# Kernel optimization log

Hardware: AMD Instinct MI355X
Metric: run time of the kernel (lower is better)

## Reference

```python
import jax, jax.numpy as jnp
import numpy as np

B, N, C = 4, 2048, 512
H = 8
HD = C // H  # 64
SCALE = HD ** -0.5


def setup_inputs() -> dict:
    key = jax.random.key(0)
    k1, k2, k3 = jax.random.split(key, 3)
    x = jax.random.normal(k1, (B, N, C), dtype=jnp.float32)
    w_qkv = jax.random.normal(k2, (3 * C, C), dtype=jnp.float32) * (C ** -0.5)
    b_qkv = jnp.zeros((3 * C,), dtype=jnp.float32)
    w_proj = jax.random.normal(k3, (C, C), dtype=jnp.float32) * (C ** -0.5)
    b_proj = jnp.zeros((C,), dtype=jnp.float32)
    return {"x": x, "w_qkv": w_qkv, "b_qkv": b_qkv, "w_proj": w_proj, "b_proj": b_proj}


def reference(x, w_qkv, b_qkv, w_proj, b_proj):
    # qkv projection: (B,N,C) @ (C,3C) -> (B,N,3,H,HD) -> (3,B,H,N,HD)
    qkv = (x @ w_qkv.T + b_qkv).reshape(B, N, 3, H, HD).transpose(2, 0, 3, 1, 4)
    q, k, v = qkv[0], qkv[1], qkv[2]
    # scores (B,H,N,N), scale applied after matmul as in the torch source
    attn = jnp.einsum('bhnd,bhmd->bhnm', q, k) * SCALE
    attn = jax.nn.softmax(attn, axis=-1)
    out = jnp.einsum('bhnm,bhmd->bhnd', attn, v)  # (B,H,N,HD)
    out = out.transpose(0, 2, 1, 3).reshape(B, N, C)
    return out @ w_proj.T + b_proj
```

## Files before the change

### kernel.cpp

```cpp
#include <hip/hip_runtime.h>

#define B_ 4
#define N_ 2048
#define C_ 512
#define H_ 8
#define HD_ 64
#define SCALE_ 0.125f
#define QSCALE_ 0.18033688011112042f

typedef __attribute__((ext_vector_type(8))) __bf16 bf16x8;
typedef __attribute__((ext_vector_type(4))) float f32x4;
typedef __attribute__((ext_vector_type(4))) unsigned int u32x4;

__device__ __forceinline__ unsigned short f2bf(float f) {
    unsigned int u = __builtin_bit_cast(unsigned int, f);
    u += 0x7fffu + ((u >> 16) & 1u);
    return (unsigned short)(u >> 16);
}

__device__ __forceinline__ void llds16(const void* g, void* l) {
    __builtin_amdgcn_global_load_lds(
        (const __attribute__((address_space(1))) unsigned int*)g,
        (__attribute__((address_space(3))) unsigned int*)l, 16, 0, 0);
}

__global__ __launch_bounds__(256) void cvt_bf16(const float* __restrict__ in,
                                                unsigned short* __restrict__ out,
                                                int n4) {
    int i = blockIdx.x * 256 + threadIdx.x;
    if (i >= n4) return;
    float4 v = ((const float4*)in)[i];
    ushort4 o;
    o.x = f2bf(v.x); o.y = f2bf(v.y); o.z = f2bf(v.z); o.w = f2bf(v.w);
    ((ushort4*)out)[i] = o;
}

template <int MODE>
__global__ __launch_bounds__(256) void gemm_bt(const unsigned short* __restrict__ A,
                                               const unsigned short* __restrict__ Bw,
                                               const float* __restrict__ bias,
                                               float* __restrict__ Out,
                                               unsigned short* __restrict__ Qb,
                                               unsigned short* __restrict__ Kb,
                                               unsigned short* __restrict__ Vt) {
    constexpr int K = 512;
    __shared__ __align__(16) unsigned char smem[32768];
    unsigned char* sA = smem;
    unsigned char* sB = smem + 16384;

    const int tid = threadIdx.x;
    const int lane = tid & 63;
    const int wave = tid >> 6;
    const int wm = wave >> 1, wn = wave & 1;
    const int m0 = blockIdx.y * 128;
    const int n0 = blockIdx.x * 128;

    f32x4 acc[4][4] = {};

    for (int k0 = 0; k0 < K; k0 += 64) {
#pragma unroll
        for (int i = 0; i < 4; i++) {
            int ci = wave * 4 + i;
            int row = ci * 8 + (lane >> 3);
            int cb = (lane & 7) * 16;
            const unsigned char* ga =
                (const unsigned char*)A + ((size_t)(m0 + row) * K + k0) * 2 + cb;
            const unsigned char* gb =
                (const unsigned char*)Bw + ((size_t)(n0 + row) * K + k0) * 2 + cb;
            llds16(ga, sA + ci * 1024);
            llds16(gb, sB + ci * 1024);
        }
        __syncthreads();
#pragma unroll
        for (int kk = 0; kk < 2; kk++) {
            bf16x8 af[4], bfr[4];
#pragma unroll
            for (int mi = 0; mi < 4; mi++)
                af[mi] = *(const bf16x8*)(sA + (wm * 64 + mi * 16 + (lane & 15)) * 128 +
                                          kk * 64 + (lane >> 4) * 16);
#pragma unroll
            for (int ni = 0; ni < 4; ni++)
                bfr[ni] = *(const bf16x8*)(sB + (wn * 64 + ni * 16 + (lane & 15)) * 128 +
                                           kk * 64 + (lane >> 4) * 16);
#pragma unroll
            for (int mi = 0; mi < 4; mi++)
#pragma unroll
                for (int ni = 0; ni < 4; ni++)
                    acc[mi][ni] = __builtin_amdgcn_mfma_f32_16x16x32_bf16(
                        af[mi], bfr[ni], acc[mi][ni], 0, 0, 0);
        }
        __syncthreads();
    }

    if constexpr (MODE == 0) {
#pragma unroll
        for (int ni = 0; ni < 4; ni++) {
            int c = n0 + wn * 64 + ni * 16 + (lane & 15);
            int sel = c >> 9, h = (c >> 6) & 7, d = c & 63;
            float bv = bias[c];
#pragma unroll
            for (int mi = 0; mi < 4; mi++) {
#pragma unroll
                for (int r = 0; r < 4; r++) {
                    int m = m0 + wm * 64 + mi * 16 + ((lane >> 4) << 2) + r;
                    int b = m >> 11, n = m & (N_ - 1);
                    float fv = acc[mi][ni][r] + bv;
                    if (sel == 0) {
                        Qb[((size_t)(b * H_ + h) * N_ + n) * HD_ + d] = f2bf(fv * QSCALE_);
                    } else if (sel == 1) {
                        Kb[((size_t)(b * H_ + h) * N_ + n) * HD_ + d] = f2bf(fv);
                    } else {
                        Vt[((size_t)(b * H_ + h) * HD_ + d) * (size_t)N_ + n] = f2bf(fv);
                    }
                }
            }
        }
    } else {
#pragma unroll
        for (int ni = 0; ni < 4; ni++) {
            int c = n0 + wn * 64 + ni * 16 + (lane & 15);
            float bv = bias[c];
#pragma unroll
            for (int mi = 0; mi < 4; mi++) {
#pragma unroll
                for (int r = 0; r < 4; r++) {
                    int m = m0 + wm * 64 + mi * 16 + ((lane >> 4) << 2) + r;
                    Out[(size_t)m * C_ + c] = acc[mi][ni][r] + bv;
                }
            }
        }
    }
}

__global__ __launch_bounds__(512, 4) void attn_fwd(const unsigned short* __restrict__ Qb,
                                                   const unsigned short* __restrict__ Kb,
                                                   const unsigned short* __restrict__ Vt,
                                                   unsigned short* __restrict__ AO) {
    __shared__ __align__(16) unsigned char smem[49152];

    const int tid = threadIdx.x, lane = tid & 63, wave = tid >> 6;
    const int bh = blockIdx.y;
    const int q0 = blockIdx.x * 128 + wave * 16;
    const unsigned short* Qh = Qb + (size_t)bh * N_ * HD_;
    const unsigned short* Kh = Kb + (size_t)bh * N_ * HD_;
    const unsigned short* Vh = Vt + (size_t)bh * HD_ * N_;
    unsigned char* sP = smem + 32768 + wave * 2048;

    bf16x8 qf[2];
#pragma unroll
    for (int kk = 0; kk < 2; kk++)
        qf[kk] = *(const bf16x8*)(Qh + (size_t)(q0 + (lane & 15)) * HD_ + kk * 32 +
                                  (lane >> 4) * 8);

    bf16x8 ones;
#pragma unroll
    for (int i = 0; i < 8; i++) ones[i] = (__bf16)1.0f;

    f32x4 o[4] = {};
    f32x4 osum = {};

    const int srow = tid >> 3;
    const int sslot = (tid & 7) * 16;
    const int ssw = (sslot ^ ((srow & 7) << 4));

    {
        u32x4 kreg = *(const u32x4*)((const unsigned char*)Kh + (size_t)srow * 128 + sslot);
        u32x4 vreg = *(const u32x4*)((const unsigned char*)Vh + (size_t)srow * (N_ * 2) + sslot);
        *(u32x4*)(smem + srow * 128 + ssw) = kreg;
        *(u32x4*)(smem + 16384 + srow * 128 + ssw) = vreg;
    }
    __syncthreads();

#pragma unroll 1
    for (int t = 0; t < N_ / 64; t++) {
        unsigned char* bK = smem + (t & 1) * 8192;
        unsigned char* bV = smem + 16384 + (t & 1) * 8192;

        u32x4 kreg, vreg;
        if (t < N_ / 64 - 1) {
            int kv0 = (t + 1) * 64;
            kreg = *(const u32x4*)((const unsigned char*)Kh + (size_t)(kv0 + srow) * 128 + sslot);
            vreg = *(const u32x4*)((const unsigned char*)Vh + (size_t)srow * (N_ * 2) +
                                   kv0 * 2 + sslot);
        }

        f32x4 s[4] = {};
#pragma unroll
        for (int j = 0; j < 4; j++) {
#pragma unroll
            for (int kk = 0; kk < 2; kk++) {
                int krow = j * 16 + (lane & 15);
                bf16x8 bf = *(const bf16x8*)(bK + krow * 128 +
                                             ((kk * 64 + (lane >> 4) * 16) ^
                                              ((krow & 7) << 4)));
                s[j] = __builtin_amdgcn_mfma_f32_16x16x32_bf16(qf[kk], bf, s[j], 0, 0, 0);
            }
        }

#pragma unroll
        for (int j = 0; j < 4; j++)
#pragma unroll
            for (int r = 0; r < 4; r++) {
                float p = __builtin_exp2f(s[j][r]);
                int row = ((lane >> 4) << 2) + r;
                int cb = (j * 16 + (lane & 15)) * 2;
                *(unsigned short*)(sP + row * 128 + (cb ^ ((row & 7) << 4))) = f2bf(p);
            }

#pragma unroll
        for (int kk = 0; kk < 2; kk++) {
            int prow = lane & 15;
            bf16x8 pf = *(const bf16x8*)(sP + prow * 128 +
                                         ((kk * 64 + (lane >> 4) * 16) ^
                                          ((prow & 7) << 4)));
            osum = __builtin_amdgcn_mfma_f32_16x16x32_bf16(pf, ones, osum, 0, 0, 0);
#pragma unroll
            for (int dj = 0; dj < 4; dj++) {
                int vrow = dj * 16 + (lane & 15);
                bf16x8 vf = *(const bf16x8*)(bV + vrow * 128 +
                                             ((kk * 64 + (lane >> 4) * 16) ^
                                              ((vrow & 7) << 4)));
                o[dj] = __builtin_amdgcn_mfma_f32_16x16x32_bf16(pf, vf, o[dj], 0, 0, 0);
            }
        }

        if (t < N_ / 64 - 1) {
            unsigned char* nK = smem + ((t + 1) & 1) * 8192;
            unsigned char* nV = smem + 16384 + ((t + 1) & 1) * 8192;
            *(u32x4*)(nK + srow * 128 + ssw) = kreg;
            *(u32x4*)(nV + srow * 128 + ssw) = vreg;
        }
        __syncthreads();
    }

    const int b = bh >> 3, h = bh & 7;
#pragma unroll
    for (int r = 0; r < 4; r++) {
        float inv = 1.0f / osum[r];
        int n = q0 + ((lane >> 4) << 2) + r;
#pragma unroll
        for (int dj = 0; dj < 4; dj++) {
            int col = h * HD_ + dj * 16 + (lane & 15);
            AO[((size_t)(b * N_ + n)) * C_ + col] = f2bf(o[dj][r] * inv);
        }
    }
}

extern "C" void kernel_launch(void* const* d_in, const int* in_sizes, int n_in,
                              void* d_out, int out_size, void* d_ws, size_t ws_size,
                              hipStream_t stream) {
    const float* x = (const float*)d_in[0];
    const float* w_qkv = (const float*)d_in[1];
    const float* b_qkv = (const float*)d_in[2];
    const float* w_proj = (const float*)d_in[3];
    const float* b_proj = (const float*)d_in[4];
    float* out = (float*)d_out;

    unsigned char* ws = (unsigned char*)d_ws;
    unsigned short* xb = (unsigned short*)ws;
    unsigned short* AO = xb;
    unsigned short* wqb = (unsigned short*)(ws + 8388608);
    unsigned short* wpb = (unsigned short*)(ws + 8388608 + 1572864);
    unsigned short* Vt = (unsigned short*)(ws + 8388608 + 1572864 + 524288);

    unsigned short* Qb = (unsigned short*)d_out;
    unsigned short* Kb = Qb + (size_t)B_ * H_ * N_ * HD_;

    cvt_bf16<<<(B_ * N_ * C_ / 4 + 255) / 256, 256, 0, stream>>>(x, xb, B_ * N_ * C_ / 4);
    cvt_bf16<<<(3 * C_ * C_ / 4 + 255) / 256, 256, 0, stream>>>(w_qkv, wqb, 3 * C_ * C_ / 4);
    cvt_bf16<<<(C_ * C_ / 4 + 255) / 256, 256, 0, stream>>>(w_proj, wpb, C_ * C_ / 4);

    gemm_bt<0><<<dim3(12, 64), 256, 0, stream>>>(xb, wqb, b_qkv, nullptr, Qb, Kb, Vt);
    attn_fwd<<<dim3(16, 32), 512, 0, stream>>>(Qb, Kb, Vt, AO);
    gemm_bt<1><<<dim3(4, 64), 256, 0, stream>>>(AO, wpb, b_proj, out, nullptr, nullptr, nullptr);
}
```

Baseline: 140.0 us.

## Fuse bf16 conversions and store P transposed, read via ds_read_tr

Merges the three fp32-to-bf16 conversion launches into one kernel to cut launch overhead. In attention, the exp'd scores are packed with v_cvt_pk_bf16_f32 and written to LDS as 64-bit stores in a transposed layout, then read back as MFMA A-operands with ds_read_b64_tr_b16. This replaces sixteen scalar 16-bit LDS stores per tile with four vector stores, at the cost of inline asm, explicit waitcnts and scheduling barriers that may limit overlap.

Result: faster. 126.6 us (-9.6%).

```diff
diff --git a/kernel.cpp b/kernel.cpp
--- a/kernel.cpp
+++ b/kernel.cpp
@@ -11,6 +11,7 @@
 typedef __attribute__((ext_vector_type(8))) __bf16 bf16x8;
 typedef __attribute__((ext_vector_type(4))) float f32x4;
 typedef __attribute__((ext_vector_type(4))) unsigned int u32x4;
+typedef __attribute__((ext_vector_type(2))) unsigned int u32x2;
 
 __device__ __forceinline__ unsigned short f2bf(float f) {
     unsigned int u = __builtin_bit_cast(unsigned int, f);
@@ -24,15 +25,25 @@
         (__attribute__((address_space(3))) unsigned int*)l, 16, 0, 0);
 }
 
-__global__ __launch_bounds__(256) void cvt_bf16(const float* __restrict__ in,
-                                                unsigned short* __restrict__ out,
-                                                int n4) {
+__global__ __launch_bounds__(256) void cvt_all(const float* __restrict__ x,
+                                               const float* __restrict__ wq,
+                                               const float* __restrict__ wp,
+                                               unsigned short* __restrict__ xb,
+                                               unsigned short* __restrict__ wqb,
+                                               unsigned short* __restrict__ wpb) {
+    const int NX = B_ * N_ * C_ / 4, NQ = 3 * C_ * C_ / 4, NP = C_ * C_ / 4;
     int i = blockIdx.x * 256 + threadIdx.x;
-    if (i >= n4) return;
-    float4 v = ((const float4*)in)[i];
+    const float4* src;
+    ushort4* dst;
+    int idx;
+    if (i < NX) { src = (const float4*)x; dst = (ushort4*)xb; idx = i; }
+    else if (i < NX + NQ) { src = (const float4*)wq; dst = (ushort4*)wqb; idx = i - NX; }
+    else if (i < NX + NQ + NP) { src = (const float4*)wp; dst = (ushort4*)wpb; idx = i - NX - NQ; }
+    else return;
+    float4 v = src[idx];
     ushort4 o;
     o.x = f2bf(v.x); o.y = f2bf(v.y); o.z = f2bf(v.z); o.w = f2bf(v.w);
-    ((ushort4*)out)[i] = o;
+    dst[idx] = o;
 }
 
 template <int MODE>
@@ -139,18 +150,20 @@
     __shared__ __align__(16) unsigned char smem[49152];
 
     const int tid = threadIdx.x, lane = tid & 63, wave = tid >> 6;
+    const int g = lane >> 4, c = lane & 15;
     const int bh = blockIdx.y;
     const int q0 = blockIdx.x * 128 + wave * 16;
     const unsigned short* Qh = Qb + (size_t)bh * N_ * HD_;
     const unsigned short* Kh = Kb + (size_t)bh * N_ * HD_;
     const unsigned short* Vh = Vt + (size_t)bh * HD_ * N_;
-    unsigned char* sP = smem + 32768 + wave * 2048;
+    unsigned char* sPT = smem + 32768 + wave * 2048;
+    unsigned char* ptw = sPT + c * 32 + g * 8;
+    const unsigned int ptr32 = (unsigned int)(size_t)sPT + g * 256 + c * 8;
 
     bf16x8 qf[2];
 #pragma unroll
     for (int kk = 0; kk < 2; kk++)
-        qf[kk] = *(const bf16x8*)(Qh + (size_t)(q0 + (lane & 15)) * HD_ + kk * 32 +
-                                  (lane >> 4) * 8);
+        qf[kk] = *(const bf16x8*)(Qh + (size_t)(q0 + c) * HD_ + kk * 32 + g * 8);
 
     bf16x8 ones;
 #pragma unroll
@@ -189,37 +202,50 @@
         for (int j = 0; j < 4; j++) {
 #pragma unroll
             for (int kk = 0; kk < 2; kk++) {
-                int krow = j * 16 + (lane & 15);
+                int krow = j * 16 + c;
                 bf16x8 bf = *(const bf16x8*)(bK + krow * 128 +
-                                             ((kk * 64 + (lane >> 4) * 16) ^
-                                              ((krow & 7) << 4)));
+                                             ((kk * 64 + g * 16) ^ ((krow & 7) << 4)));
                 s[j] = __builtin_amdgcn_mfma_f32_16x16x32_bf16(qf[kk], bf, s[j], 0, 0, 0);
             }
         }
 
 #pragma unroll
-        for (int j = 0; j < 4; j++)
-#pragma unroll
-            for (int r = 0; r < 4; r++) {
-                float p = __builtin_exp2f(s[j][r]);
-                int row = ((lane >> 4) << 2) + r;
-                int cb = (j * 16 + (lane & 15)) * 2;
-                *(unsigned short*)(sP + row * 128 + (cb ^ ((row & 7) << 4))) = f2bf(p);
-            }
+        for (int j = 0; j < 4; j++) {
+            float p0 = __builtin_exp2f(s[j][0]);
+            float p1 = __builtin_exp2f(s[j][1]);
+            float p2 = __builtin_exp2f(s[j][2]);
+            float p3 = __builtin_exp2f(s[j][3]);
+            unsigned int lo, hi;
+            asm("v_cvt_pk_bf16_f32 %0, %1, %2" : "=v"(lo) : "v"(p0), "v"(p1));
+            asm("v_cvt_pk_bf16_f32 %0, %1, %2" : "=v"(hi) : "v"(p2), "v"(p3));
+            u32x2 w;
+            w[0] = lo;
+            w[1] = hi;
+            *(u32x2*)(ptw + j * 512) = w;
+        }
+
+        asm volatile("s_waitcnt lgkmcnt(0)" ::: "memory");
+        __builtin_amdgcn_sched_barrier(0);
 
 #pragma unroll
         for (int kk = 0; kk < 2; kk++) {
-            int prow = lane & 15;
-            bf16x8 pf = *(const bf16x8*)(sP + prow * 128 +
-                                         ((kk * 64 + (lane >> 4) * 16) ^
-                                          ((prow & 7) << 4)));
+            u32x2 t0, t1;
+            asm volatile("ds_read_b64_tr_b16 %0, %2\n\t"
+                         "ds_read_b64_tr_b16 %1, %2 offset:128"
+                         : "=v"(t0), "=v"(t1)
+                         : "v"(ptr32 + kk * 1024)
+                         : "memory");
+            asm volatile("s_waitcnt lgkmcnt(0)");
+            __builtin_amdgcn_sched_barrier(0);
+            u32x4 wq;
+            wq[0] = t0[0]; wq[1] = t0[1]; wq[2] = t1[0]; wq[3] = t1[1];
+            bf16x8 pf = __builtin_bit_cast(bf16x8, wq);
             osum = __builtin_amdgcn_mfma_f32_16x16x32_bf16(pf, ones, osum, 0, 0, 0);
 #pragma unroll
             for (int dj = 0; dj < 4; dj++) {
-                int vrow = dj * 16 + (lane & 15);
+                int vrow = dj * 16 + c;
                 bf16x8 vf = *(const bf16x8*)(bV + vrow * 128 +
-                                             ((kk * 64 + (lane >> 4) * 16) ^
-                                              ((vrow & 7) << 4)));
+                                             ((kk * 64 + g * 16) ^ ((vrow & 7) << 4)));
                 o[dj] = __builtin_amdgcn_mfma_f32_16x16x32_bf16(pf, vf, o[dj], 0, 0, 0);
             }
         }
@@ -237,10 +263,10 @@
 #pragma unroll
     for (int r = 0; r < 4; r++) {
         float inv = 1.0f / osum[r];
-        int n = q0 + ((lane >> 4) << 2) + r;
+        int n = q0 + (g << 2) + r;
 #pragma unroll
         for (int dj = 0; dj < 4; dj++) {
-            int col = h * HD_ + dj * 16 + (lane & 15);
+            int col = h * HD_ + dj * 16 + c;
             AO[((size_t)(b * N_ + n)) * C_ + col] = f2bf(o[dj][r] * inv);
         }
     }
@@ -266,9 +292,8 @@
     unsigned short* Qb = (unsigned short*)d_out;
     unsigned short* Kb = Qb + (size_t)B_ * H_ * N_ * HD_;
 
-    cvt_bf16<<<(B_ * N_ * C_ / 4 + 255) / 256, 256, 0, stream>>>(x, xb, B_ * N_ * C_ / 4);
-    cvt_bf16<<<(3 * C_ * C_ / 4 + 255) / 256, 256, 0, stream>>>(w_qkv, wqb, 3 * C_ * C_ / 4);
-    cvt_bf16<<<(C_ * C_ / 4 + 255) / 256, 256, 0, stream>>>(w_proj, wpb, C_ * C_ / 4);
+    const int NALL = (B_ * N_ * C_ + 3 * C_ * C_ + C_ * C_) / 4;
+    cvt_all<<<(NALL + 255) / 256, 256, 0, stream>>>(x, w_qkv, w_proj, xb, wqb, wpb);
 
     gemm_bt<0><<<dim3(12, 64), 256, 0, stream>>>(xb, wqb, b_qkv, nullptr, Qb, Kb, Vt);
     attn_fwd<<<dim3(16, 32), 512, 0, stream>>>(Qb, Kb, Vt, AO);
```
